# Kernel tuning notes

Hardware: AMD Instinct MI355X
Metric: run time of the kernel (lower is better)

The kernel has to match this reference:

```python
import jax, jax.numpy as jnp
import numpy as np

B, N, E = 16, 2048, 1_048_576          # graphs, residues per graph, total edges
IN_C, DIM, OUT_C, ENC_H, N_ATOMS = 256, 128, 6, 100, 20
NT = B * N


def setup_inputs() -> dict:
    key = jax.random.key(0)
    ks = jax.random.split(key, 24)
    s = 0.02
    x_res = jax.random.normal(ks[0], (NT, IN_C), jnp.float32)
    coords = jax.random.normal(ks[1], (NT, 3), jnp.float32)
    batch = jnp.repeat(jnp.arange(B, dtype=jnp.int32), N)
    src = jax.random.randint(ks[2], (E,), 0, NT, dtype=jnp.int32)
    dst = (src // N) * N + jax.random.randint(ks[3], (E,), 0, N, dtype=jnp.int32)
    edge_index = jnp.stack([src, dst])  # intra-graph edges, global node ids
    return {
        'x_res': x_res, 'coords': coords,
        'edge_index': edge_index, 'batch': batch,
        'bn_gamma': jnp.ones((IN_C,), jnp.float32),
        'bn_beta': jnp.zeros((IN_C,), jnp.float32),
        'W1': s * jax.random.normal(ks[4], (IN_C, 2 * DIM), jnp.float32),
        'b1': jnp.zeros((2 * DIM,), jnp.float32),
        'W2': s * jax.random.normal(ks[5], (2 * DIM, DIM), jnp.float32),
        'b2': jnp.zeros((DIM,), jnp.float32),
        'W3': s * jax.random.normal(ks[6], (DIM, N_ATOMS), jnp.float32),
        'b3': jnp.zeros((N_ATOMS,), jnp.float32),
        'embed': s * jax.random.normal(ks[7], (N_ATOMS + 1, DIM), jnp.float32),
        'W_msg': s * jax.random.normal(ks[8], (DIM, DIM), jnp.float32),
        'b_msg': jnp.zeros((DIM,), jnp.float32),
        'w_coor': s * jax.random.normal(ks[9], (DIM, 3), jnp.float32),
        'A1': s * jax.random.normal(ks[10], (DIM, ENC_H), jnp.float32),
        'a1': jnp.zeros((ENC_H,), jnp.float32),
        'A2': s * jax.random.normal(ks[11], (ENC_H, OUT_C), jnp.float32),
        'a2': jnp.zeros((OUT_C,), jnp.float32),
        'dyt_alpha': jnp.float32(0.5),
        'dyt_w': jnp.ones((OUT_C,), jnp.float32),
        'dyt_b': jnp.zeros((OUT_C,), jnp.float32),
    }


def reference(x_res, coords, edge_index, batch,
              bn_gamma, bn_beta, W1, b1, W2, b2, W3, b3,
              embed, W_msg, b_msg, w_coor,
              A1, a1, A2, a2, dyt_alpha, dyt_w, dyt_b):
    gelu = lambda v: jax.nn.gelu(v, approximate=False)
    # BatchNorm1d (train-mode batch stats, biased var, eps=1e-5); dropout is identity in eval
    mu = x_res.mean(0)
    var = x_res.var(0)
    xn = (x_res - mu) / jnp.sqrt(var + 1e-5) * bn_gamma + bn_beta
    # input2atomids MLP -> argmax atom ids
    h1 = gelu(xn @ W1 + b1)
    h2 = gelu(h1 @ W2 + b2)
    logits = h2 @ W3 + b3
    ids = jnp.argmax(logits, axis=-1)          # [NT]
    ids_b = ids.reshape(B, N)                  # equal-sized graphs -> no padding needed
    coords_b = coords.reshape(B, N, 3)
    # vectorized edge-list -> dense per-graph adjacency scatter
    g = batch[edge_index[0]]                   # graph id per edge
    ls = edge_index[0] - g * N                 # local src index
    ld = edge_index[1] - g * N                 # local dst index
    same = batch[edge_index[1]] == g           # keep intra-graph edges only
    adj = jnp.zeros((B, N, N), jnp.bool_).at[g, ls, ld].max(same)
    # GotenNet stand-in: embed atom ids, one adjacency-masked aggregation layer
    emb_ids = jnp.where(ids_b < 0, N_ATOMS, ids_b)   # -1 pad -> pad embedding row
    h = embed[emb_ids]                          # [B,N,DIM]
    adjf = adj.astype(h.dtype)
    deg = jnp.maximum(adjf.sum(-1, keepdims=True), 1.0)
    m = jnp.einsum('bij,bjd->bid', adjf, h) / deg
    hout = gelu((h + m) @ W_msg + b_msg)        # invariant features [B,N,DIM]
    coors_out = coords_b + jnp.tanh(hout @ w_coor)
    # un-pad / flatten back to node list, then out_angles head
    z = hout.reshape(NT, DIM)
    t = gelu(z @ A1 + a1)
    t = gelu(t @ A2 + a2)
    t = jnp.tanh(dyt_alpha * t) * dyt_w + dyt_b  # DynamicTanh (channels_last)
    angles = jnp.tanh(t)                         # [NT, OUT_C]
    return angles, z, coors_out
```

## Files before the change

### kernel.cpp

```cpp
#include <hip/hip_runtime.h>
#include <hip/hip_bf16.h>
#include <math.h>

#define Bg 16
#define Nn 2048
#define Ee (1<<20)
#define NT (Bg*Nn)
#define INC 256
#define DIMd 128
#define OUTC 6
#define ENCH 100
#define NATOMS 20
#define BINCAP 3072

typedef __attribute__((ext_vector_type(8))) short bf16x8;
typedef __attribute__((ext_vector_type(4))) float f32x4;

__device__ __forceinline__ float gelu_f(float x){
    return 0.5f*x*(1.0f+erff(x*0.70710678118654752440f));
}
__device__ __forceinline__ unsigned short f2b(float f){
    __hip_bfloat16 h = __float2bfloat16(f);
    return *(unsigned short*)&h;
}
__device__ __forceinline__ float b2f(unsigned short u){
    unsigned v = ((unsigned)u)<<16;
    return __uint_as_float(v);
}
__device__ __forceinline__ void splitf(float v, unsigned short& hi, unsigned short& lo){
    unsigned short h = f2b(v);
    hi = h; lo = f2b(v - b2f(h));
}

__global__ __launch_bounds__(256) void prep0_k(const float* __restrict__ x,
    float* __restrict__ stats, const float* __restrict__ W1,
    const float* __restrict__ W2, const float* __restrict__ Wm,
    const float* __restrict__ A1, short* __restrict__ w1th, short* __restrict__ w1tl,
    short* __restrict__ w2th, short* __restrict__ w2tl,
    short* __restrict__ wmth, short* __restrict__ wmtl,
    short* __restrict__ a1th, short* __restrict__ a1tl)
{
    int bx = blockIdx.x, tid = threadIdx.x;
    if(bx < 256){
        int c = tid;
        int r0 = bx * 128;
        const float* p = x + (size_t)r0*INC + c;
        float s = 0.f, s2 = 0.f;
        #pragma unroll 8
        for(int r=0;r<128;r++){ float v = p[(size_t)r*INC]; s += v; s2 += v*v; }
        atomicAdd(&stats[c], s);
        atomicAdd(&stats[INC+c], s2);
    } else {
        int gid = (bx-256)*256 + tid;
        unsigned short hi, lo;
        for(int l=gid;l<65536;l+=16384){ int n=l>>8,k=l&255;
            splitf(W1[(size_t)k*256+n],hi,lo); w1th[l]=(short)hi; w1tl[l]=(short)lo; }
        for(int l=gid;l<32768;l+=16384){ int n=l>>8,k=l&255;
            splitf(W2[(size_t)k*128+n],hi,lo); w2th[l]=(short)hi; w2tl[l]=(short)lo; }
        for(int l=gid;l<16384;l+=16384){ int n=l>>7,k=l&127;
            splitf(Wm[(size_t)k*128+n],hi,lo); wmth[l]=(short)hi; wmtl[l]=(short)lo; }
        for(int l=gid;l<16384;l+=16384){ int n=l>>7,k=l&127;
            float v=(n<ENCH)? A1[(size_t)k*ENCH+n] : 0.f;
            splitf(v,hi,lo); a1th[l]=(short)hi; a1tl[l]=(short)lo; }
    }
}

__global__ __launch_bounds__(256) void gemm123_k(const float* __restrict__ x,
    const float* __restrict__ stats, const float* __restrict__ gamma,
    const float* __restrict__ beta, const short* __restrict__ w1th,
    const short* __restrict__ w1tl, const float* __restrict__ b1,
    const short* __restrict__ w2th, const short* __restrict__ w2tl,
    const float* __restrict__ b2, const float* __restrict__ W3,
    const float* __restrict__ b3, int* __restrict__ ids,
    const int* __restrict__ ei, unsigned* __restrict__ ecnt,
    unsigned* __restrict__ earena)
{
    __shared__ float sc[256], sh[256];
    __shared__ __align__(16) unsigned char smem[51200];
    short* sAh = (short*)smem;
    short* sAl = sAh + 64*40;
    short* sBh = (short*)(smem + 10240);
    short* sBl = sBh + 256*40;
    float* h2s = (float*)(smem + 10240);
    float* lgs = (float*)(smem + 44032);
    float* w3s = (float*)smem;

    int tid = threadIdx.x;
    {
        float mu  = stats[tid]*(1.0f/NT);
        float var = stats[256+tid]*(1.0f/NT) - mu*mu;
        float s = gamma[tid]/sqrtf(var + 1e-5f);
        sc[tid] = s; sh[tid] = beta[tid] - mu*s;
    }
    int row0 = blockIdx.x*64;
    int lane = tid&63, w = tid>>6;
    int ln = lane&15, quad = lane>>4;
    int m0w = (w&1)*32, nb1 = (w>>1)*128, nb2 = (w>>1)*64;

    f32x4 acc[2][8];
    #pragma unroll
    for(int i=0;i<2;i++)
        #pragma unroll
        for(int j=0;j<8;j++) acc[i][j] = (f32x4){0.f,0.f,0.f,0.f};
    float bias1[8];
    #pragma unroll
    for(int tn=0;tn<8;tn++) bias1[tn] = b1[nb1 + tn*16 + ln];

    float4 xa[2]; bf16x8 wb[8];
    #pragma unroll
    for(int i=0;i<2;i++){ int id=tid+i*256; int r=id>>3,kq=(id&7)*4;
        xa[i] = *(const float4*)&x[(size_t)(row0+r)*256 + kq]; }
    #pragma unroll
    for(int i=0;i<8;i++){ int id=tid+i*256; int plane=id>>10,cid=id&1023;
        int r=cid>>2,c=cid&3;
        wb[i] = *(const bf16x8*)((plane? w1tl:w1th) + (size_t)r*256 + c*8); }
    __syncthreads();
    for(int k0=0;k0<256;k0+=32){
        #pragma unroll
        for(int i=0;i<2;i++){
            int id = tid + i*256; int r = id>>3, kq = (id&7)*4;
            int k = k0+kq;
            float v0 = xa[i].x*sc[k]+sh[k],     v1 = xa[i].y*sc[k+1]+sh[k+1];
            float v2 = xa[i].z*sc[k+2]+sh[k+2], v3 = xa[i].w*sc[k+3]+sh[k+3];
            ushort4 hi, lo;
            splitf(v0,hi.x,lo.x); splitf(v1,hi.y,lo.y);
            splitf(v2,hi.z,lo.z); splitf(v3,hi.w,lo.w);
            *(ushort4*)&sAh[r*40+kq] = hi;
            *(ushort4*)&sAl[r*40+kq] = lo;
        }
        #pragma unroll
        for(int i=0;i<8;i++){
            int id = tid + i*256; int plane = id>>10, cid = id&1023;
            int r = cid>>2, c = cid&3;
            *(bf16x8*)((plane? sBl : sBh) + r*40 + c*8) = wb[i];
        }
        __syncthreads();
        if(k0 < 224){
            #pragma unroll
            for(int i=0;i<2;i++){ int id=tid+i*256; int r=id>>3,kq=(id&7)*4;
                xa[i] = *(const float4*)&x[(size_t)(row0+r)*256 + k0+32+kq]; }
            #pragma unroll
            for(int i=0;i<8;i++){ int id=tid+i*256; int plane=id>>10,cid=id&1023;
                int r=cid>>2,c=cid&3;
                wb[i] = *(const bf16x8*)((plane? w1tl:w1th) + (size_t)r*256 + k0+32 + c*8); }
        }
        bf16x8 ah[2], al[2];
        #pragma unroll
        for(int tm=0;tm<2;tm++){
            ah[tm] = *(const bf16x8*)&sAh[(m0w+tm*16+ln)*40 + quad*8];
            al[tm] = *(const bf16x8*)&sAl[(m0w+tm*16+ln)*40 + quad*8];
        }
        #pragma unroll
        for(int tn=0;tn<8;tn++){
            bf16x8 bh = *(const bf16x8*)&sBh[(nb1+tn*16+ln)*40 + quad*8];
            bf16x8 bl = *(const bf16x8*)&sBl[(nb1+tn*16+ln)*40 + quad*8];
            #pragma unroll
            for(int tm=0;tm<2;tm++){
                acc[tm][tn] = __builtin_amdgcn_mfma_f32_16x16x32_bf16(al[tm], bh, acc[tm][tn], 0,0,0);
                acc[tm][tn] = __builtin_amdgcn_mfma_f32_16x16x32_bf16(ah[tm], bl, acc[tm][tn], 0,0,0);
                acc[tm][tn] = __builtin_amdgcn_mfma_f32_16x16x32_bf16(ah[tm], bh, acc[tm][tn], 0,0,0);
            }
        }
        __syncthreads();
    }

    f32x4 acc2[2][4];
    #pragma unroll
    for(int i=0;i<2;i++)
        #pragma unroll
        for(int j=0;j<4;j++) acc2[i][j] = (f32x4){0.f,0.f,0.f,0.f};
    bf16x8 wb2[4];
    #pragma unroll
    for(int i=0;i<4;i++){ int id=tid+i*256; int plane=id>>9,cid=id&511;
        int r=cid>>2,c=cid&3;
        wb2[i] = *(const bf16x8*)((plane? w2tl:w2th) + (size_t)r*256 + c*8); }
    #pragma unroll
    for(int cc=0;cc<8;cc++){
        if((w>>1) == (cc>>2)){
            int clp = cc&3;
            #pragma unroll
            for(int t=0;t<2;t++){
                int tn = 2*clp + t;
                #pragma unroll
                for(int tm=0;tm<2;tm++){
                    #pragma unroll
                    for(int r=0;r<4;r++){
                        int row = m0w + tm*16 + quad*4 + r;
                        float hv = gelu_f(acc[tm][tn][r] + bias1[tn]);
                        unsigned short hi, lo;
                        splitf(hv, hi, lo);
                        sAh[row*40 + t*16 + ln] = (short)hi;
                        sAl[row*40 + t*16 + ln] = (short)lo;
                    }
                }
            }
        }
        #pragma unroll
        for(int i=0;i<4;i++){
            int id = tid + i*256; int plane = id>>9, cid = id&511;
            int r = cid>>2, c = cid&3;
            *(bf16x8*)((plane? sBl : sBh) + r*40 + c*8) = wb2[i];
        }
        __syncthreads();
        if(cc < 7){
            #pragma unroll
            for(int i=0;i<4;i++){ int id=tid+i*256; int plane=id>>9,cid=id&511;
                int r=cid>>2,c=cid&3;
                wb2[i] = *(const bf16x8*)((plane? w2tl:w2th)
                          + (size_t)r*256 + (cc+1)*32 + c*8); }
        }
        bf16x8 ah[2], al[2];
        #pragma unroll
        for(int tm=0;tm<2;tm++){
            ah[tm] = *(const bf16x8*)&sAh[(m0w+tm*16+ln)*40 + quad*8];
            al[tm] = *(const bf16x8*)&sAl[(m0w+tm*16+ln)*40 + quad*8];
        }
        #pragma unroll
        for(int tn=0;tn<4;tn++){
            bf16x8 bh = *(const bf16x8*)&sBh[(nb2+tn*16+ln)*40 + quad*8];
            bf16x8 bl = *(const bf16x8*)&sBl[(nb2+tn*16+ln)*40 + quad*8];
            #pragma unroll
            for(int tm=0;tm<2;tm++){
                acc2[tm][tn] = __builtin_amdgcn_mfma_f32_16x16x32_bf16(al[tm], bh, acc2[tm][tn], 0,0,0);
                acc2[tm][tn] = __builtin_amdgcn_mfma_f32_16x16x32_bf16(ah[tm], bl, acc2[tm][tn], 0,0,0);
                acc2[tm][tn] = __builtin_amdgcn_mfma_f32_16x16x32_bf16(ah[tm], bh, acc2[tm][tn], 0,0,0);
            }
        }
        __syncthreads();
    }

    #pragma unroll
    for(int tn=0;tn<4;tn++){
        int col = nb2 + tn*16 + ln;
        float bias = b2[col];
        #pragma unroll
        for(int tm=0;tm<2;tm++){
            int rb = m0w + tm*16 + quad*4;
            #pragma unroll
            for(int r=0;r<4;r++)
                h2s[(rb+r)*132 + col] = gelu_f(acc2[tm][tn][r] + bias);
        }
    }
    for(int l=tid;l<2560;l+=256) w3s[l] = W3[l];
    __syncthreads();
    {
        int n = tid>>2, q = tid&3;
        float lg[5] = {};
        #pragma unroll 4
        for(int k=0;k<128;k++){
            float h = h2s[n*132+k];
            #pragma unroll
            for(int a=0;a<5;a++) lg[a] += h*w3s[k*20 + q*5 + a];
        }
        #pragma unroll
        for(int a=0;a<5;a++) lgs[n*20 + q*5 + a] = lg[a] + b3[q*5+a];
    }
    __syncthreads();
    if(tid<64){
        float best = lgs[tid*20]; int bi = 0;
        #pragma unroll
        for(int a=1;a<20;a++){ float v2 = lgs[tid*20+a]; if(v2>best){best=v2;bi=a;} }
        ids[row0+tid] = bi;
    }

    if(blockIdx.x < 256){
        __syncthreads();
        unsigned* lcnt  = (unsigned*)sAh;
        unsigned* gbase = ((unsigned*)sAh) + 512;
        for(int l=tid; l<512; l+=256) lcnt[l] = 0;
        __syncthreads();
        int ebase = blockIdx.x * 4096;
        #pragma unroll 4
        for(int i=0;i<16;i++){
            int e = ebase + i*256 + tid;
            int s = ei[e], d = ei[Ee+e];
            if((s>>11)==(d>>11)) atomicAdd(&lcnt[s>>6], 1u);
        }
        __syncthreads();
        for(int l=tid; l<512; l+=256){
            unsigned c = lcnt[l];
            gbase[l] = c ? atomicAdd(&ecnt[l], c) : 0u;
            lcnt[l] = 0;
        }
        __syncthreads();
        #pragma unroll 4
        for(int i=0;i<16;i++){
            int e = ebase + i*256 + tid;
            int s = ei[e], d = ei[Ee+e];
            if((s>>11)==(d>>11)){
                int bin = s>>6;
                unsigned r = atomicAdd(&lcnt[bin], 1u);
                unsigned pos = gbase[bin] + r;
                if(pos < BINCAP)
                    earena[(size_t)bin*BINCAP + pos] =
                        ((unsigned)(s&63)<<11) | (unsigned)(d&2047);
            }
        }
    }
}

__global__ __launch_bounds__(256) void msg3_k(
    const int* __restrict__ ids, const unsigned* __restrict__ ecnt,
    const unsigned* __restrict__ earena, const float* __restrict__ embed,
    const short* __restrict__ wmth, const short* __restrict__ wmtl,
    const float* __restrict__ b_msg, const float* __restrict__ w_coor,
    const short* __restrict__ a1th, const short* __restrict__ a1tl,
    const float* __restrict__ a1v, const float* __restrict__ A2,
    const float* __restrict__ a2v, const float* __restrict__ dalpha,
    const float* __restrict__ dw, const float* __restrict__ db,
    const float* __restrict__ coords, float* __restrict__ out_ang,
    float* __restrict__ out_z, float* __restrict__ out_co)
{
    __shared__ unsigned short v_bf[64*136];
    __shared__ unsigned short houts[64*136];
    __shared__ __align__(16) unsigned char arena[33792];
    __shared__ float s_bm[128], s_wc[384], s_A2[624], s_a1[104];
    __shared__ float s_dyt[16], s_a2[8];

    unsigned*       lmask = (unsigned*)arena;
    unsigned*       ind   = (unsigned*)(arena + 16384);
    unsigned char*  sid   = arena + 21504;
    float*          emb   = (float*)(arena + 23552);
    short*          sBh   = (short*)arena;
    short*          sBl   = (short*)(arena + 10240);

    int tid = threadIdx.x;
    int bin = blockIdx.x;
    int row0 = bin*64;
    int g = blockIdx.x>>5, tile = blockIdx.x&31;
    int lane = tid&63, w = tid>>6;
    int ln = lane&15, quad = lane>>4;
    int m0w = (w&1)*32, n0w = (w>>1)*64;

    for(int l=tid;l<NATOMS*128;l+=256) emb[l] = embed[l];
    #pragma unroll
    for(int i=0;i<8;i++){ int j = tid + i*256; sid[j] = (unsigned char)ids[g*Nn + j]; }
    #pragma unroll
    for(int i=0;i<16;i++) lmask[tid + i*256] = 0;
    if(tid<128) s_bm[tid] = b_msg[tid];
    if(tid<104) s_a1[tid] = (tid<ENCH) ? a1v[tid] : 0.f;
    for(int l=tid;l<384;l+=256) s_wc[l] = w_coor[l];
    for(int l=tid;l<624;l+=256) s_A2[l] = (l<600) ? A2[l] : 0.f;
    if(tid==0)  s_dyt[0] = dalpha[0];
    if(tid<6){ s_dyt[1+tid] = dw[tid]; s_dyt[8+tid] = db[tid]; }
    if(tid<8)  s_a2[tid] = (tid<6) ? a2v[tid] : 0.f;
    int nb = min((int)ecnt[bin], BINCAP);
    __syncthreads();

    for(int wp=w; wp<32; wp+=4){
        int a = sid[wp*64 + lane];
        #pragma unroll
        for(int atom=0; atom<NATOMS; atom++){
            unsigned long long bm = __ballot(a==atom);
            if(lane<2) ind[atom*64 + wp*2 + lane] = (unsigned)(bm >> (32*lane));
        }
    }
    for(int i=tid; i<nb; i+=256){
        unsigned wv = earena[(size_t)bin*BINCAP + i];
        int sl = wv>>11, dl = wv & 2047;
        atomicOr(&lmask[sl*64 + (dl>>5)], 1u<<(dl&31));
    }
    __syncthreads();

    int node = tid>>2, p = tid&3;
    unsigned mw[16];
    {
        const unsigned* mrow = &lmask[node*64 + p*16];
        *(uint4*)&mw[0]  = *(const uint4*)&mrow[0];
        *(uint4*)&mw[4]  = *(const uint4*)&mrow[4];
        *(uint4*)&mw[8]  = *(const uint4*)&mrow[8];
        *(uint4*)&mw[12] = *(const uint4*)&mrow[12];
    }
    int degi = 0;
    #pragma unroll
    for(int w2=0;w2<16;w2++) degi += __popc(mw[w2]);
    float cnt[NATOMS];
    #pragma unroll
    for(int a=0;a<NATOMS;a++){
        int c = 0;
        const unsigned* ia = &ind[a*64 + p*16];
        #pragma unroll
        for(int w2=0;w2<16;w2++) c += __popc(mw[w2] & ia[w2]);
        cnt[a] = (float)c;
    }
    #pragma unroll
    for(int a=0;a<NATOMS;a++){
        cnt[a] += __shfl_xor(cnt[a],1,64);
        cnt[a] += __shfl_xor(cnt[a],2,64);
    }
    float deg = (float)degi;
    deg += __shfl_xor(deg,1,64);
    deg += __shfl_xor(deg,2,64);

    {
        float inv = 1.0f / fmaxf(deg, 1.0f);
        int oid = sid[tile*64 + node];
        int d0 = p*32;
        float vv[32];
        #pragma unroll
        for(int d=0;d<32;d++) vv[d]=0.f;
        #pragma unroll
        for(int a=0;a<NATOMS;a++){
            float ca = cnt[a];
            const float* ea = &emb[a*128 + d0];
            #pragma unroll
            for(int d=0;d<32;d+=4){
                float4 e = *(const float4*)&ea[d];
                vv[d]+=ca*e.x; vv[d+1]+=ca*e.y; vv[d+2]+=ca*e.z; vv[d+3]+=ca*e.w;
            }
        }
        const float* eo = &emb[oid*128 + d0];
        unsigned short* dst = &v_bf[node*136 + d0];
        #pragma unroll
        for(int d=0;d<32;d+=4){
            float4 e = *(const float4*)&eo[d];
            ushort4 o;
            o.x = f2b(e.x + vv[d]*inv);
            o.y = f2b(e.y + vv[d+1]*inv);
            o.z = f2b(e.z + vv[d+2]*inv);
            o.w = f2b(e.w + vv[d+3]*inv);
            *(ushort4*)&dst[d] = o;
        }
    }
    __syncthreads();

    f32x4 acc[2][4];
    #pragma unroll
    for(int i=0;i<2;i++)
        #pragma unroll
        for(int j=0;j<4;j++) acc[i][j] = (f32x4){0.f,0.f,0.f,0.f};
    for(int k0=0;k0<128;k0+=32){
        #pragma unroll
        for(int i=0;i<4;i++){
            int id = tid + i*256; int plane = id>>9, cid = id&511;
            int r = cid>>2, c = cid&3;
            const short* src = (plane? wmtl : wmth) + (size_t)r*128 + k0 + c*8;
            short* dst = (plane? sBl : sBh) + r*40 + c*8;
            *(bf16x8*)dst = *(const bf16x8*)src;
        }
        __syncthreads();
        bf16x8 av[2];
        #pragma unroll
        for(int tm=0;tm<2;tm++)
            av[tm] = *(const bf16x8*)&v_bf[(m0w+tm*16+ln)*136 + k0 + quad*8];
        #pragma unroll
        for(int tn=0;tn<4;tn++){
            bf16x8 bh = *(const bf16x8*)&sBh[(n0w+tn*16+ln)*40 + quad*8];
            bf16x8 bl = *(const bf16x8*)&sBl[(n0w+tn*16+ln)*40 + quad*8];
            #pragma unroll
            for(int tm=0;tm<2;tm++){
                acc[tm][tn] = __builtin_amdgcn_mfma_f32_16x16x32_bf16(av[tm], bl, acc[tm][tn], 0,0,0);
                acc[tm][tn] = __builtin_amdgcn_mfma_f32_16x16x32_bf16(av[tm], bh, acc[tm][tn], 0,0,0);
            }
        }
        __syncthreads();
    }
    #pragma unroll
    for(int tn=0;tn<4;tn++){
        int col = n0w + tn*16 + ln;
        float bias = s_bm[col];
        #pragma unroll
        for(int tm=0;tm<2;tm++){
            int mb2 = m0w + tm*16 + quad*4;
            #pragma unroll
            for(int r=0;r<4;r++){
                float hv = gelu_f(acc[tm][tn][r] + bias);
                out_z[(size_t)(row0+mb2+r)*128 + col] = hv;
                houts[(mb2+r)*136 + col] = f2b(hv);
            }
        }
    }
    __syncthreads();

    {
        float d0=0.f, d1=0.f, d2=0.f;
        int kb = p*32;
        #pragma unroll
        for(int k=0;k<32;k+=4){
            ushort4 hv = *(const ushort4*)&houts[node*136 + kb + k];
            float h0=b2f(hv.x),h1=b2f(hv.y),h2=b2f(hv.z),h3=b2f(hv.w);
            const float* wc = &s_wc[(kb+k)*3];
            d0 += h0*wc[0]+h1*wc[3]+h2*wc[6]+h3*wc[9];
            d1 += h0*wc[1]+h1*wc[4]+h2*wc[7]+h3*wc[10];
            d2 += h0*wc[2]+h1*wc[5]+h2*wc[8]+h3*wc[11];
        }
        d0 += __shfl_xor(d0,1,64); d0 += __shfl_xor(d0,2,64);
        d1 += __shfl_xor(d1,1,64); d1 += __shfl_xor(d1,2,64);
        d2 += __shfl_xor(d2,1,64); d2 += __shfl_xor(d2,2,64);
        if(p==0){
            size_t o = (size_t)(row0+node)*3;
            out_co[o+0] = coords[o+0] + tanhf(d0);
            out_co[o+1] = coords[o+1] + tanhf(d1);
            out_co[o+2] = coords[o+2] + tanhf(d2);
        }
    }

    f32x4 acc2[2][4];
    #pragma unroll
    for(int i=0;i<2;i++)
        #pragma unroll
        for(int j=0;j<4;j++) acc2[i][j] = (f32x4){0.f,0.f,0.f,0.f};
    for(int k0=0;k0<128;k0+=32){
        __syncthreads();
        #pragma unroll
        for(int i=0;i<4;i++){
            int id = tid + i*256; int plane = id>>9, cid = id&511;
            int r = cid>>2, c = cid&3;
            const short* src = (plane? a1tl : a1th) + (size_t)r*128 + k0 + c*8;
            short* dst = (plane? sBl : sBh) + r*40 + c*8;
            *(bf16x8*)dst = *(const bf16x8*)src;
        }
        __syncthreads();
        bf16x8 ah[2];
        #pragma unroll
        for(int tm=0;tm<2;tm++)
            ah[tm] = *(const bf16x8*)&houts[(m0w+tm*16+ln)*136 + k0 + quad*8];
        #pragma unroll
        for(int tn=0;tn<4;tn++){
            bf16x8 bh = *(const bf16x8*)&sBh[(n0w+tn*16+ln)*40 + quad*8];
            bf16x8 bl = *(const bf16x8*)&sBl[(n0w+tn*16+ln)*40 + quad*8];
            #pragma unroll
            for(int tm=0;tm<2;tm++){
                acc2[tm][tn] = __builtin_amdgcn_mfma_f32_16x16x32_bf16(ah[tm], bl, acc2[tm][tn], 0,0,0);
                acc2[tm][tn] = __builtin_amdgcn_mfma_f32_16x16x32_bf16(ah[tm], bh, acc2[tm][tn], 0,0,0);
            }
        }
    }
    __syncthreads();
    unsigned short* t1s = houts;
    #pragma unroll
    for(int tn=0;tn<4;tn++){
        int col = n0w + tn*16 + ln;
        if(col < 104){
            float bias = s_a1[col];
            #pragma unroll
            for(int tm=0;tm<2;tm++){
                int mb2 = m0w + tm*16 + quad*4;
                #pragma unroll
                for(int r=0;r<4;r++)
                    t1s[(mb2+r)*104 + col] = f2b(gelu_f(acc2[tm][tn][r] + bias));
            }
        }
    }
    __syncthreads();

    {
        int g0 = (p<2) ? p*7 : 14+(p-2)*6;
        int gcount = (p<2) ? 7 : 6;
        float s[6] = {0.f,0.f,0.f,0.f,0.f,0.f};
        for(int gg=0; gg<gcount; gg++){
            int kb = (g0+gg)*4;
            ushort4 tv = *(const ushort4*)&t1s[node*104 + kb];
            float u0=b2f(tv.x), u1=b2f(tv.y), u2=b2f(tv.z), u3=b2f(tv.w);
            #pragma unroll
            for(int j=0;j<6;j++)
                s[j] += u0*s_A2[kb*6+j] + u1*s_A2[(kb+1)*6+j]
                      + u2*s_A2[(kb+2)*6+j] + u3*s_A2[(kb+3)*6+j];
        }
        #pragma unroll
        for(int j=0;j<6;j++){ s[j]+=__shfl_xor(s[j],1,64); s[j]+=__shfl_xor(s[j],2,64); }
        if(p<2){
            size_t o = (size_t)(row0+node)*6 + p*3;
            #pragma unroll
            for(int jj=0;jj<3;jj++){
                int j = p*3+jj;
                float t2v = gelu_f(s[j] + s_a2[j]);
                float uu = tanhf(s_dyt[0]*t2v)*s_dyt[1+j] + s_dyt[8+j];
                out_ang[o+jj] = tanhf(uu);
            }
        }
    }
}

extern "C" void kernel_launch(void* const* d_in, const int* in_sizes, int n_in,
                              void* d_out, int out_size, void* d_ws, size_t ws_size,
                              hipStream_t stream) {
    const float* x      = (const float*)d_in[0];
    const float* coords = (const float*)d_in[1];
    const int*   ei     = (const int*)d_in[2];
    const float* gamma  = (const float*)d_in[4];
    const float* beta   = (const float*)d_in[5];
    const float* W1     = (const float*)d_in[6];
    const float* b1     = (const float*)d_in[7];
    const float* W2     = (const float*)d_in[8];
    const float* b2     = (const float*)d_in[9];
    const float* W3     = (const float*)d_in[10];
    const float* b3     = (const float*)d_in[11];
    const float* embed  = (const float*)d_in[12];
    const float* W_msg  = (const float*)d_in[13];
    const float* b_msg  = (const float*)d_in[14];
    const float* w_coor = (const float*)d_in[15];
    const float* A1     = (const float*)d_in[16];
    const float* a1v    = (const float*)d_in[17];
    const float* A2     = (const float*)d_in[18];
    const float* a2v    = (const float*)d_in[19];
    const float* dalpha = (const float*)d_in[20];
    const float* dw     = (const float*)d_in[21];
    const float* db     = (const float*)d_in[22];

    char* ws = (char*)d_ws;
    int*      ids   = (int*)ws;
    float*    stats = (float*)(ws + 131072);
    unsigned* ecnt  = (unsigned*)(ws + 131072 + 2048);
    short*    w1th  = (short*)(ws + 262144);
    short*    w1tl  = w1th + 65536;
    short*    w2th  = w1tl + 65536;
    short*    w2tl  = w2th + 32768;
    short*    wmth  = w2tl + 32768;
    short*    wmtl  = wmth + 16384;
    short*    a1th  = wmtl + 16384;
    short*    a1tl  = a1th + 16384;
    unsigned* earena = (unsigned*)(ws + (1<<20));

    float* out_ang = (float*)d_out;
    float* out_z   = out_ang + (size_t)NT*OUTC;
    float* out_co  = out_z   + (size_t)NT*DIMd;

    hipMemsetAsync(stats, 0, 4096, stream);
    prep0_k<<<320, 256, 0, stream>>>(x, stats, W1, W2, W_msg, A1,
        w1th, w1tl, w2th, w2tl, wmth, wmtl, a1th, a1tl);
    gemm123_k<<<512, 256, 0, stream>>>(x, stats, gamma, beta, w1th, w1tl, b1,
        w2th, w2tl, b2, W3, b3, ids, ei, ecnt, earena);
    msg3_k<<<512, 256, 0, stream>>>(ids, ecnt, earena, embed, wmth, wmtl, b_msg,
        w_coor, a1th, a1tl, a1v, A2, a2v, dalpha, dw, db, coords,
        out_ang, out_z, out_co);
}
```

Baseline: 268.1 us.

## Tile weight transpose via LDS and deepen register prefetch in GEMM loops

The weight split/transpose in prep0 now stages 64x64 tiles through padded shared memory, so both the global reads and the bf16 writes are coalesced, and the launch uses fewer blocks. The first GEMM loop in gemm123 prefetches two K-steps ahead with double-buffered registers. msg3 preloads its edge words into registers, hoists the bin-count read, and register-prefetches the Wmsg and A1 weight slices ahead of their shared-memory stores. This hides global latency at the cost of more register pressure, which may lower occupancy.

```diff
diff --git a/kernel.cpp b/kernel.cpp
--- a/kernel.cpp
+++ b/kernel.cpp
@@ -40,6 +40,7 @@
     short* __restrict__ wmth, short* __restrict__ wmtl,
     short* __restrict__ a1th, short* __restrict__ a1tl)
 {
+    __shared__ float st[64*65];
     int bx = blockIdx.x, tid = threadIdx.x;
     if(bx < 256){
         int c = tid;
@@ -50,18 +51,33 @@
         for(int r=0;r<128;r++){ float v = p[(size_t)r*INC]; s += v; s2 += v*v; }
         atomicAdd(&stats[c], s);
         atomicAdd(&stats[INC+c], s2);
-    } else {
-        int gid = (bx-256)*256 + tid;
+        return;
+    }
+    int t = bx - 256;
+    const float* src; short *dh, *dl;
+    int k0, n0, lds, ldd, nmax;
+    if(t < 16){        src=W1; dh=w1th; dl=w1tl; lds=256; ldd=256; nmax=256;
+                       k0=(t>>2)*64;      n0=(t&3)*64; }
+    else if(t < 24){   int u=t-16; src=W2; dh=w2th; dl=w2tl; lds=128; ldd=256; nmax=128;
+                       k0=(u>>1)*64;      n0=(u&1)*64; }
+    else if(t < 28){   int u=t-24; src=Wm; dh=wmth; dl=wmtl; lds=128; ldd=128; nmax=128;
+                       k0=(u>>1)*64;      n0=(u&1)*64; }
+    else {             int u=t-28; src=A1; dh=a1th; dl=a1tl; lds=100; ldd=128; nmax=100;
+                       k0=(u>>1)*64;      n0=(u&1)*64; }
+    #pragma unroll
+    for(int i=0;i<16;i++){
+        int idx = tid + i*256; int r = idx>>6, c = idx&63;
+        float v = (n0+c < nmax) ? src[(size_t)(k0+r)*lds + n0+c] : 0.f;
+        st[r*65+c] = v;
+    }
+    __syncthreads();
+    #pragma unroll
+    for(int i=0;i<16;i++){
+        int idx = tid + i*256; int rr = idx>>6, cc = idx&63;
         unsigned short hi, lo;
-        for(int l=gid;l<65536;l+=16384){ int n=l>>8,k=l&255;
-            splitf(W1[(size_t)k*256+n],hi,lo); w1th[l]=(short)hi; w1tl[l]=(short)lo; }
-        for(int l=gid;l<32768;l+=16384){ int n=l>>8,k=l&255;
-            splitf(W2[(size_t)k*128+n],hi,lo); w2th[l]=(short)hi; w2tl[l]=(short)lo; }
-        for(int l=gid;l<16384;l+=16384){ int n=l>>7,k=l&127;
-            splitf(Wm[(size_t)k*128+n],hi,lo); wmth[l]=(short)hi; wmtl[l]=(short)lo; }
-        for(int l=gid;l<16384;l+=16384){ int n=l>>7,k=l&127;
-            float v=(n<ENCH)? A1[(size_t)k*ENCH+n] : 0.f;
-            splitf(v,hi,lo); a1th[l]=(short)hi; a1tl[l]=(short)lo; }
+        splitf(st[cc*65+rr], hi, lo);
+        size_t o = (size_t)(n0+rr)*ldd + k0+cc;
+        dh[o] = (short)hi; dl[o] = (short)lo;
     }
 }
 
@@ -106,22 +122,26 @@
     #pragma unroll
     for(int tn=0;tn<8;tn++) bias1[tn] = b1[nb1 + tn*16 + ln];
 
-    float4 xa[2]; bf16x8 wb[8];
-    #pragma unroll
-    for(int i=0;i<2;i++){ int id=tid+i*256; int r=id>>3,kq=(id&7)*4;
-        xa[i] = *(const float4*)&x[(size_t)(row0+r)*256 + kq]; }
-    #pragma unroll
-    for(int i=0;i<8;i++){ int id=tid+i*256; int plane=id>>10,cid=id&1023;
-        int r=cid>>2,c=cid&3;
-        wb[i] = *(const bf16x8*)((plane? w1tl:w1th) + (size_t)r*256 + c*8); }
+    float4 xa[2][2]; bf16x8 wb[2][8];
+    #pragma unroll
+    for(int t=0;t<2;t++){
+        #pragma unroll
+        for(int i=0;i<2;i++){ int id=tid+i*256; int r=id>>3,kq=(id&7)*4;
+            xa[t][i] = *(const float4*)&x[(size_t)(row0+r)*256 + t*32 + kq]; }
+        #pragma unroll
+        for(int i=0;i<8;i++){ int id=tid+i*256; int plane=id>>10,cid=id&1023;
+            int r=cid>>2,c=cid&3;
+            wb[t][i] = *(const bf16x8*)((plane? w1tl:w1th) + (size_t)r*256 + t*32 + c*8); }
+    }
     __syncthreads();
     for(int k0=0;k0<256;k0+=32){
+        int cur = (k0>>5)&1;
         #pragma unroll
         for(int i=0;i<2;i++){
             int id = tid + i*256; int r = id>>3, kq = (id&7)*4;
             int k = k0+kq;
-            float v0 = xa[i].x*sc[k]+sh[k],     v1 = xa[i].y*sc[k+1]+sh[k+1];
-            float v2 = xa[i].z*sc[k+2]+sh[k+2], v3 = xa[i].w*sc[k+3]+sh[k+3];
+            float v0 = xa[cur][i].x*sc[k]+sh[k],     v1 = xa[cur][i].y*sc[k+1]+sh[k+1];
+            float v2 = xa[cur][i].z*sc[k+2]+sh[k+2], v3 = xa[cur][i].w*sc[k+3]+sh[k+3];
             ushort4 hi, lo;
             splitf(v0,hi.x,lo.x); splitf(v1,hi.y,lo.y);
             splitf(v2,hi.z,lo.z); splitf(v3,hi.w,lo.w);
@@ -132,17 +152,17 @@
         for(int i=0;i<8;i++){
             int id = tid + i*256; int plane = id>>10, cid = id&1023;
             int r = cid>>2, c = cid&3;
-            *(bf16x8*)((plane? sBl : sBh) + r*40 + c*8) = wb[i];
-        }
-        __syncthreads();
-        if(k0 < 224){
+            *(bf16x8*)((plane? sBl : sBh) + r*40 + c*8) = wb[cur][i];
+        }
+        __syncthreads();
+        if(k0 < 192){
             #pragma unroll
             for(int i=0;i<2;i++){ int id=tid+i*256; int r=id>>3,kq=(id&7)*4;
-                xa[i] = *(const float4*)&x[(size_t)(row0+r)*256 + k0+32+kq]; }
+                xa[cur][i] = *(const float4*)&x[(size_t)(row0+r)*256 + k0+64+kq]; }
             #pragma unroll
             for(int i=0;i<8;i++){ int id=tid+i*256; int plane=id>>10,cid=id&1023;
                 int r=cid>>2,c=cid&3;
-                wb[i] = *(const bf16x8*)((plane? w1tl:w1th) + (size_t)r*256 + k0+32 + c*8); }
+                wb[cur][i] = *(const bf16x8*)((plane? w1tl:w1th) + (size_t)r*256 + k0+64 + c*8); }
         }
         bf16x8 ah[2], al[2];
         #pragma unroll
@@ -332,6 +352,7 @@
     int ln = lane&15, quad = lane>>4;
     int m0w = (w&1)*32, n0w = (w>>1)*64;
 
+    int nb = min((int)ecnt[bin], BINCAP);
     for(int l=tid;l<NATOMS*128;l+=256) emb[l] = embed[l];
     #pragma unroll
     for(int i=0;i<8;i++){ int j = tid + i*256; sid[j] = (unsigned char)ids[g*Nn + j]; }
@@ -344,9 +365,14 @@
     if(tid==0)  s_dyt[0] = dalpha[0];
     if(tid<6){ s_dyt[1+tid] = dw[tid]; s_dyt[8+tid] = db[tid]; }
     if(tid<8)  s_a2[tid] = (tid<6) ? a2v[tid] : 0.f;
-    int nb = min((int)ecnt[bin], BINCAP);
-    __syncthreads();
-
+    __syncthreads();
+
+    unsigned ew[12]; int ne = 0;
+    #pragma unroll
+    for(int j=0;j<12;j++){
+        int i = tid + j*256;
+        if(i < nb){ ew[j] = earena[(size_t)bin*BINCAP + i]; ne = j+1; }
+    }
     for(int wp=w; wp<32; wp+=4){
         int a = sid[wp*64 + lane];
         #pragma unroll
@@ -355,13 +381,18 @@
             if(lane<2) ind[atom*64 + wp*2 + lane] = (unsigned)(bm >> (32*lane));
         }
     }
-    for(int i=tid; i<nb; i+=256){
-        unsigned wv = earena[(size_t)bin*BINCAP + i];
+    for(int j=0;j<ne;j++){
+        unsigned wv = ew[j];
         int sl = wv>>11, dl = wv & 2047;
         atomicOr(&lmask[sl*64 + (dl>>5)], 1u<<(dl&31));
     }
     __syncthreads();
 
+    bf16x8 wbm[4];
+    #pragma unroll
+    for(int i=0;i<4;i++){ int id=tid+i*256; int plane=id>>9,cid=id&511;
+        int r=cid>>2,c=cid&3;
+        wbm[i] = *(const bf16x8*)((plane? wmtl:wmth) + (size_t)r*128 + c*8); }
     int node = tid>>2, p = tid&3;
     unsigned mw[16];
     {
@@ -434,11 +465,16 @@
         for(int i=0;i<4;i++){
             int id = tid + i*256; int plane = id>>9, cid = id&511;
             int r = cid>>2, c = cid&3;
-            const short* src = (plane? wmtl : wmth) + (size_t)r*128 + k0 + c*8;
-            short* dst = (plane? sBl : sBh) + r*40 + c*8;
-            *(bf16x8*)dst = *(const bf16x8*)src;
-        }
-        __syncthreads();
+            *(bf16x8*)((plane? sBl : sBh) + r*40 + c*8) = wbm[i];
+        }
+        __syncthreads();
+        if(k0 < 96){
+            #pragma unroll
+            for(int i=0;i<4;i++){ int id=tid+i*256; int plane=id>>9,cid=id&511;
+                int r=cid>>2,c=cid&3;
+                wbm[i] = *(const bf16x8*)((plane? wmtl:wmth)
+                          + (size_t)r*128 + k0+32 + c*8); }
+        }
         bf16x8 av[2];
         #pragma unroll
         for(int tm=0;tm<2;tm++)
@@ -455,6 +491,11 @@
         }
         __syncthreads();
     }
+    bf16x8 wa[4];
+    #pragma unroll
+    for(int i=0;i<4;i++){ int id=tid+i*256; int plane=id>>9,cid=id&511;
+        int r=cid>>2,c=cid&3;
+        wa[i] = *(const bf16x8*)((plane? a1tl:a1th) + (size_t)r*128 + c*8); }
     #pragma unroll
     for(int tn=0;tn<4;tn++){
         int col = n0w + tn*16 + ln;
@@ -506,11 +547,16 @@
         for(int i=0;i<4;i++){
             int id = tid + i*256; int plane = id>>9, cid = id&511;
             int r = cid>>2, c = cid&3;
-            const short* src = (plane? a1tl : a1th) + (size_t)r*128 + k0 + c*8;
-            short* dst = (plane? sBl : sBh) + r*40 + c*8;
-            *(bf16x8*)dst = *(const bf16x8*)src;
-        }
-        __syncthreads();
+            *(bf16x8*)((plane? sBl : sBh) + r*40 + c*8) = wa[i];
+        }
+        __syncthreads();
+        if(k0 < 96){
+            #pragma unroll
+            for(int i=0;i<4;i++){ int id=tid+i*256; int plane=id>>9,cid=id&511;
+                int r=cid>>2,c=cid&3;
+                wa[i] = *(const bf16x8*)((plane? a1tl:a1th)
+                          + (size_t)r*128 + k0+32 + c*8); }
+        }
         bf16x8 ah[2];
         #pragma unroll
         for(int tm=0;tm<2;tm++)
@@ -617,7 +663,7 @@
     float* out_co  = out_z   + (size_t)NT*DIMd;
 
     hipMemsetAsync(stats, 0, 4096, stream);
-    prep0_k<<<320, 256, 0, stream>>>(x, stats, W1, W2, W_msg, A1,
+    prep0_k<<<288, 256, 0, stream>>>(x, stats, W1, W2, W_msg, A1,
         w1th, w1tl, w2th, w2tl, wmth, wmtl, a1th, a1tl);
     gemm123_k<<<512, 256, 0, stream>>>(x, stats, gamma, beta, w1th, w1tl, b1,
         w2th, w2tl, b2, W3, b3, ids, ei, ecnt, earena);
```

New measurement: 261.3 us. 1.03x faster.
